# Optimization experiments

Hardware: AMD Instinct MI355X
Metric: run time of the kernel (lower is better)

## Reference

```python
import jax, jax.numpy as jnp
import numpy as np

N_NODES = 100000
N_EDGES = 250000
LATENT = 128
N_FEAT = 16
OUT = 128


def _mlp(x, W1, b1, W2, b2, W3, b3):
    # per-(class, port) MLP xi^{c,o}: two relu hidden layers, linear output
    h = jax.nn.relu(x @ W1 + b1)
    h = jax.nn.relu(h @ W2 + b2)
    return h @ W3 + b3


def setup_inputs() -> dict:
    key = jax.random.key(0)
    ks = jax.random.split(key, 12)
    d_in = 2 * LATENT + N_FEAT  # 272
    s = lambda k, shp, fan: jax.random.normal(k, shp, jnp.float32) / np.sqrt(fan)
    return {
        "coordinates": jax.random.normal(ks[0], (N_NODES, LATENT), jnp.float32),
        "edge_features": jax.random.normal(ks[1], (N_EDGES, N_FEAT), jnp.float32),
        "non_fictitious": jnp.ones((N_EDGES,), jnp.float32),
        "addr_port1": jax.random.randint(ks[2], (N_EDGES,), 0, N_NODES, jnp.int32),
        "addr_port2": jax.random.randint(ks[3], (N_EDGES,), 0, N_NODES, jnp.int32),
        "p1_W1": s(ks[4], (d_in, 256), d_in), "p1_b1": jnp.zeros((256,), jnp.float32),
        "p1_W2": s(ks[5], (256, 256), 256), "p1_b2": jnp.zeros((256,), jnp.float32),
        "p1_W3": s(ks[6], (256, OUT), 256), "p1_b3": jnp.zeros((OUT,), jnp.float32),
        "p2_W1": s(ks[7], (d_in, 256), d_in), "p2_b1": jnp.zeros((256,), jnp.float32),
        "p2_W2": s(ks[8], (256, 256), 256), "p2_b2": jnp.zeros((256,), jnp.float32),
        "p2_W3": s(ks[9], (256, OUT), 256), "p2_b3": jnp.zeros((OUT,), jnp.float32),
    }


def reference(coordinates, edge_features, non_fictitious, addr_port1, addr_port2,
              p1_W1, p1_b1, p1_W2, p1_b2, p1_W3, p1_b3,
              p2_W1, p2_b1, p2_W2, p2_b2, p2_W3, p2_b3):
    # Gather neighbor coordinates for each port and concat with edge features.
    # input_array: [n_edges, n_feat + 2*latent]
    inp = jnp.concatenate(
        [edge_features, coordinates[addr_port1], coordinates[addr_port2]], axis=-1)
    mask = non_fictitious[:, None]  # [n_edges, 1]

    acc = jnp.zeros((coordinates.shape[0], OUT), dtype=coordinates.dtype)
    # port 1 MLP -> scatter-add at port-1 addresses
    acc = acc.at[addr_port1].add(_mlp(inp, p1_W1, p1_b1, p1_W2, p1_b2, p1_W3, p1_b3) * mask)
    # port 2 MLP -> scatter-add at port-2 addresses
    acc = acc.at[addr_port2].add(_mlp(inp, p2_W1, p2_b1, p2_W2, p2_b2, p2_W3, p2_b3) * mask)
    return jnp.tanh(acc)
```

## Files before the change

### kernel.cpp

```cpp
#include <hip/hip_runtime.h>
#include <cstdint>

#define N_NODES 100000
#define N_EDGES_C 250000
#define LATENT 128
#define N_FEAT 16
#define OUT_DIM 128
#define D_IN 272
#define KC1 9
#define KC2 8
#define NT1 16
#define NT2 16
#define NT3 8
#define EPB 64
#define MT 4

#define SZ1 (KC1*NT1*512)
#define SZ2 (KC2*NT2*512)
#define SZ3 (KC2*NT3*512)
#define SZ_MLP (SZ1+SZ2+SZ3)
#define SZ_ALL (2*SZ_MLP)
#define WBLK (SZ_ALL/256)

#define NC4 (N_NODES*LATENT/4)
#define NE4 (N_EDGES_C*N_FEAT/4)
#define CBLK ((NC4+NE4+255)/256)

typedef _Float16 f16;
typedef _Float16 f16x8 __attribute__((ext_vector_type(8)));
typedef float f32x4 __attribute__((ext_vector_type(4)));
typedef unsigned short u16;
typedef u16 u16x8 __attribute__((ext_vector_type(8)));

__device__ u16 g_coords_h[(size_t)N_NODES * LATENT];
__device__ u16 g_efeat_h[(size_t)N_EDGES_C * N_FEAT];

static __device__ __forceinline__ u16 f16_bits(float v) {
    f16 h = (f16)v;
    return __builtin_bit_cast(u16, h);
}

__global__ void prep_all(const float* __restrict__ W1a, const float* __restrict__ W2a,
                         const float* __restrict__ W3a, const float* __restrict__ W1b,
                         const float* __restrict__ W2b, const float* __restrict__ W3b,
                         const float* __restrict__ coords, const float* __restrict__ efeat,
                         u16* __restrict__ Whi) {
    if (blockIdx.x < WBLK) {
        int idx = blockIdx.x * 256 + threadIdx.x;
        int mlp = idx / SZ_MLP;
        int r = idx - mlp * SZ_MLP;
        const float* Wsrc; int NT, Kreal, N, rl;
        if (r < SZ1)            { Wsrc = mlp ? W1b : W1a; NT = NT1; Kreal = D_IN; N = 256; rl = r; }
        else if (r < SZ1 + SZ2) { Wsrc = mlp ? W2b : W2a; NT = NT2; Kreal = 256;  N = 256; rl = r - SZ1; }
        else                    { Wsrc = mlp ? W3b : W3a; NT = NT3; Kreal = 256;  N = 128; rl = r - SZ1 - SZ2; }
        int block  = rl >> 9;
        int within = rl & 511;
        int quad = within >> 7;
        int nn   = (within >> 3) & 15;
        int j    = within & 7;
        int c = block / NT;
        int t = block - c * NT;
        int k = c * 32 + quad * 8 + j;
        int n = t * 16 + nn;
        float w = (k < Kreal) ? Wsrc[(size_t)k * N + n] : 0.f;
        Whi[idx] = f16_bits(w);
    } else {
        int i = (blockIdx.x - WBLK) * 256 + threadIdx.x;
        const float* src;
        u16* dst;
        if (i < NC4)               { src = coords + (size_t)i * 4; dst = g_coords_h + (size_t)i * 4; }
        else if (i < NC4 + NE4)    { int j = i - NC4; src = efeat + (size_t)j * 4; dst = g_efeat_h + (size_t)j * 4; }
        else return;
        f32x4 v = *(const f32x4*)src;
        ushort4 h;
        h.x = f16_bits(v.x); h.y = f16_bits(v.y);
        h.z = f16_bits(v.z); h.w = f16_bits(v.w);
        *(ushort4*)dst = h;
    }
}

static __device__ __forceinline__ void gatherX(u16* __restrict__ A,
                                               const int* __restrict__ pA,
                                               const int* __restrict__ pB,
                                               int ebase, int tid) {
    int m = tid >> 3;
    int p = tid & 7;
    int e = ebase + m;
    bool v = e < N_EDGES_C;
    int i1 = pA[m];
    int i2 = pB[m];
    const u16* ef = g_efeat_h + (size_t)e * N_FEAT;
    const u16* c1 = g_coords_h + (size_t)i1 * LATENT;
    const u16* c2 = g_coords_h + (size_t)i2 * LATENT;
    int mt = m >> 4, mr = m & 15;
    #pragma unroll
    for (int it = 0; it < 5; ++it) {
        int ci = p + it * 8;
        if (ci >= 36) break;
        int k = ci * 8;
        u16x8 h;
        if (!v || k >= D_IN)  h = (u16x8){0, 0, 0, 0, 0, 0, 0, 0};
        else if (k < 16)      h = __builtin_nontemporal_load((const u16x8*)(ef + k));
        else if (k < 144)     h = __builtin_nontemporal_load((const u16x8*)(c1 + (k - 16)));
        else                  h = __builtin_nontemporal_load((const u16x8*)(c2 + (k - 144)));
        int chunk = k >> 5, quad = (k >> 3) & 3;
        *(u16x8*)&A[(mt * KC1 + chunk) * 512 + quad * 128 + mr * 8] = h;
    }
}

template<int KCL, int KCA, int CT, int NTT>
static __device__ __forceinline__ void kloop(const u16* __restrict__ A,
                                             const u16* __restrict__ W,
                                             int w4, int lane,
                                             f32x4 (&acc)[MT][CT]) {
    const int la8 = lane * 8;
    const int tg0 = w4 * CT;
    u16x8 b[CT];
    #pragma unroll
    for (int t = 0; t < CT; ++t)
        b[t] = *(const u16x8*)&W[(tg0 + t) * 512 + la8];
    #pragma unroll
    for (int c = 0; c < KCL; ++c) {
        u16x8 bn[CT];
        if (c + 1 < KCL) {
            #pragma unroll
            for (int t = 0; t < CT; ++t)
                bn[t] = *(const u16x8*)&W[((c + 1) * NTT + tg0 + t) * 512 + la8];
        }
        f16x8 a[MT];
        #pragma unroll
        for (int mt = 0; mt < MT; ++mt)
            a[mt] = __builtin_bit_cast(f16x8, *(const u16x8*)&A[(mt * KCA + c) * 512 + la8]);
        #pragma unroll
        for (int t = 0; t < CT; ++t) {
            f16x8 bf = __builtin_bit_cast(f16x8, b[t]);
            #pragma unroll
            for (int mt = 0; mt < MT; ++mt)
                acc[mt][t] = __builtin_amdgcn_mfma_f32_16x16x32_f16(a[mt], bf, acc[mt][t], 0, 0, 0);
        }
        if (c + 1 < KCL) {
            #pragma unroll
            for (int t = 0; t < CT; ++t) b[t] = bn[t];
        }
    }
}

template<int KCL, int KCA, int CT, int NTT>
static __device__ __forceinline__ void layer_mm(const u16* __restrict__ A,
                                                const u16* __restrict__ W,
                                                int w4, int lane,
                                                f32x4 (&acc)[MT][CT]) {
    #pragma unroll
    for (int mt = 0; mt < MT; ++mt)
        #pragma unroll
        for (int t = 0; t < CT; ++t)
            acc[mt][t] = (f32x4){0.f, 0.f, 0.f, 0.f};
    kloop<KCL, KCA, CT, NTT>(A, W, w4, lane, acc);
}

template<int CT>
static __device__ __forceinline__ void epi_relu(u16* __restrict__ H,
                                                const float* __restrict__ bias,
                                                int w4, int lane,
                                                f32x4 (&acc)[MT][CT]) {
    int quad = lane >> 4, ln = lane & 15;
    #pragma unroll
    for (int t = 0; t < CT; ++t) {
        int n = (w4 * CT + t) * 16 + ln;
        float b = bias[n];
        int chunk = n >> 5, q2 = (n >> 3) & 3, j = n & 7;
        #pragma unroll
        for (int mt = 0; mt < MT; ++mt)
            #pragma unroll
            for (int r = 0; r < 4; ++r) {
                float v = acc[mt][t][r] + b;
                v = fmaxf(v, 0.f);
                H[(mt * KC2 + chunk) * 512 + q2 * 128 + (quad * 4 + r) * 8 + j] = f16_bits(v);
            }
    }
}

__global__ void __launch_bounds__(512, 4)
fused_mlp(const float* __restrict__ nfict,
          const int* __restrict__ port1, const int* __restrict__ port2,
          const float* __restrict__ b1a, const float* __restrict__ b2a, const float* __restrict__ b3a,
          const float* __restrict__ b1b, const float* __restrict__ b2b, const float* __restrict__ b3b,
          const u16* __restrict__ Whi,
          float* __restrict__ out) {
    __shared__ u16 X[MT * KC1 * 512];
    __shared__ u16 Ha[MT * KC2 * 512];
    __shared__ int pA[EPB], pB[EPB];
    __shared__ float mk[EPB];

    const int tid = threadIdx.x;
    const int lane = tid & 63;
    const int wave = tid >> 6;
    const int ebase = blockIdx.x * EPB;

    if (tid < EPB) {
        int e = ebase + tid;
        bool v = e < N_EDGES_C;
        pA[tid] = v ? port1[e] : 0;
        pB[tid] = v ? port2[e] : 0;
        mk[tid] = v ? nfict[e] : 0.f;
    }
    __syncthreads();
    gatherX(X, pA, pB, ebase, tid);
    __syncthreads();

    const int msel = wave >> 2;
    const int w4 = wave & 3;
    const u16* wh = Whi + msel * SZ_MLP;
    const float* B1 = msel ? b1b : b1a;
    const float* B2 = msel ? b2b : b2a;
    const float* B3 = msel ? b3b : b3a;
    const int*   pp = msel ? pB  : pA;
    u16* myH = msel ? X : Ha;

    f32x4 acc[MT][4];
    layer_mm<KC1, KC1, 4, NT1>(X, wh, w4, lane, acc);
    __syncthreads();
    epi_relu<4>(myH, B1, w4, lane, acc);
    __syncthreads();

    layer_mm<KC2, KC2, 4, NT2>(myH, wh + SZ1, w4, lane, acc);
    __syncthreads();
    epi_relu<4>(myH, B2, w4, lane, acc);
    __syncthreads();

    f32x4 acc3[MT][2];
    layer_mm<KC2, KC2, 2, NT3>(myH, wh + SZ1 + SZ2, w4, lane, acc3);

    int quad = lane >> 4, ln = lane & 15;
    #pragma unroll
    for (int t = 0; t < 2; ++t) {
        int n = (w4 * 2 + t) * 16 + ln;
        float bz = B3[n];
        #pragma unroll
        for (int mt = 0; mt < MT; ++mt)
            #pragma unroll
            for (int r = 0; r < 4; ++r) {
                int m = mt * 16 + quad * 4 + r;
                float v = (acc3[mt][t][r] + bz) * mk[m];
                unsafeAtomicAdd(out + (size_t)pp[m] * OUT_DIM + n, v);
            }
    }
}

__global__ void tanh_kernel(float* __restrict__ out, int n) {
    int i = (blockIdx.x * 256 + threadIdx.x) * 4;
    if (i + 3 < n) {
        float4 v = *(float4*)(out + i);
        v.x = tanhf(v.x); v.y = tanhf(v.y); v.z = tanhf(v.z); v.w = tanhf(v.w);
        *(float4*)(out + i) = v;
    } else {
        for (int k = i; k < n; ++k) out[k] = tanhf(out[k]);
    }
}

extern "C" void kernel_launch(void* const* d_in, const int* in_sizes, int n_in,
                              void* d_out, int out_size, void* d_ws, size_t ws_size,
                              hipStream_t stream) {
    const float* coords = (const float*)d_in[0];
    const float* efeat  = (const float*)d_in[1];
    const float* nfict  = (const float*)d_in[2];
    const int*   p1     = (const int*)d_in[3];
    const int*   p2     = (const int*)d_in[4];
    const float* W1a = (const float*)d_in[5];  const float* b1a = (const float*)d_in[6];
    const float* W2a = (const float*)d_in[7];  const float* b2a = (const float*)d_in[8];
    const float* W3a = (const float*)d_in[9];  const float* b3a = (const float*)d_in[10];
    const float* W1b = (const float*)d_in[11]; const float* b1b = (const float*)d_in[12];
    const float* W2b = (const float*)d_in[13]; const float* b2b = (const float*)d_in[14];
    const float* W3b = (const float*)d_in[15]; const float* b3b = (const float*)d_in[16];
    float* out = (float*)d_out;
    u16* Whi = (u16*)d_ws;

    hipMemsetAsync(d_out, 0, (size_t)out_size * sizeof(float), stream);
    prep_all<<<WBLK + CBLK, 256, 0, stream>>>(W1a, W2a, W3a, W1b, W2b, W3b,
                                              coords, efeat, Whi);
    int nblk = (N_EDGES_C + EPB - 1) / EPB;
    fused_mlp<<<nblk, 512, 0, stream>>>(nfict, p1, p2,
                                        b1a, b2a, b3a, b1b, b2b, b3b, Whi, out);
    int n4 = (out_size + 3) / 4;
    tanh_kernel<<<(n4 + 255) / 256, 256, 0, stream>>>(out, out_size);
}
```

Baseline: 499.4 us.

## Replace atomic scatter-add with CSR segmented reduction fused with tanh

The MLP kernel now writes per-edge messages to a global buffer instead of issuing float atomics into the output. A counting sort (count, single-block scan, fill) builds a per-node list of message rows, and a new kernel sums each node's messages with one wave per node and applies tanh, which replaces the memset and the separate tanh pass. This removes atomic contention and the extra output traffic. In exchange it writes and rereads about 256 MB of messages and adds several small launches, including a serial single-block scan.

```diff
diff --git a/kernel.cpp b/kernel.cpp
--- a/kernel.cpp
+++ b/kernel.cpp
@@ -25,6 +25,10 @@
 #define NC4 (N_NODES*LATENT/4)
 #define NE4 (N_EDGES_C*N_FEAT/4)
 #define CBLK ((NC4+NE4+255)/256)
+#define ZBLK ((N_NODES+255)/256)
+
+#define MSG_STRIDE 250048
+#define MSG_ROWS   (2*MSG_STRIDE)
 
 typedef _Float16 f16;
 typedef _Float16 f16x8 __attribute__((ext_vector_type(8)));
@@ -32,8 +36,13 @@
 typedef unsigned short u16;
 typedef u16 u16x8 __attribute__((ext_vector_type(8)));
 
-__device__ u16 g_coords_h[(size_t)N_NODES * LATENT];
-__device__ u16 g_efeat_h[(size_t)N_EDGES_C * N_FEAT];
+__device__ u16   g_coords_h[(size_t)N_NODES * LATENT];
+__device__ u16   g_efeat_h[(size_t)N_EDGES_C * N_FEAT];
+__device__ float g_msg[(size_t)MSG_ROWS * OUT_DIM];
+__device__ int   g_cnt[N_NODES];
+__device__ int   g_off[N_NODES];
+__device__ int   g_cur[N_NODES];
+__device__ int   g_eidx[2 * N_EDGES_C];
 
 static __device__ __forceinline__ u16 f16_bits(float v) {
     f16 h = (f16)v;
@@ -64,7 +73,7 @@
         int n = t * 16 + nn;
         float w = (k < Kreal) ? Wsrc[(size_t)k * N + n] : 0.f;
         Whi[idx] = f16_bits(w);
-    } else {
+    } else if (blockIdx.x < WBLK + CBLK) {
         int i = (blockIdx.x - WBLK) * 256 + threadIdx.x;
         const float* src;
         u16* dst;
@@ -76,7 +85,56 @@
         h.x = f16_bits(v.x); h.y = f16_bits(v.y);
         h.z = f16_bits(v.z); h.w = f16_bits(v.w);
         *(ushort4*)dst = h;
-    }
+    } else {
+        int i = (blockIdx.x - WBLK - CBLK) * 256 + threadIdx.x;
+        if (i < N_NODES) g_cnt[i] = 0;
+    }
+}
+
+__global__ void count_kernel(const int* __restrict__ port1, const int* __restrict__ port2) {
+    int i = blockIdx.x * 256 + threadIdx.x;
+    if (i >= 2 * N_EDGES_C) return;
+    int node = (i < N_EDGES_C) ? port1[i] : port2[i - N_EDGES_C];
+    atomicAdd(&g_cnt[node], 1);
+}
+
+__global__ void __launch_bounds__(1024) scan_kernel() {
+    __shared__ int s[1024];
+    const int t = threadIdx.x;
+    const int CH = (N_NODES + 1023) / 1024;
+    int base = t * CH;
+    int sum = 0;
+    for (int i = 0; i < CH; ++i) {
+        int idx = base + i;
+        if (idx < N_NODES) sum += g_cnt[idx];
+    }
+    s[t] = sum;
+    __syncthreads();
+    for (int off = 1; off < 1024; off <<= 1) {
+        int u = (t >= off) ? s[t - off] : 0;
+        __syncthreads();
+        s[t] += u;
+        __syncthreads();
+    }
+    int run = s[t] - sum;
+    for (int i = 0; i < CH; ++i) {
+        int idx = base + i;
+        if (idx < N_NODES) {
+            g_off[idx] = run;
+            g_cur[idx] = run;
+            run += g_cnt[idx];
+        }
+    }
+}
+
+__global__ void fill_kernel(const int* __restrict__ port1, const int* __restrict__ port2) {
+    int i = blockIdx.x * 256 + threadIdx.x;
+    if (i >= 2 * N_EDGES_C) return;
+    int node, row;
+    if (i < N_EDGES_C) { node = port1[i]; row = i; }
+    else               { node = port2[i - N_EDGES_C]; row = i + (MSG_STRIDE - N_EDGES_C); }
+    int pos = atomicAdd(&g_cur[node], 1);
+    g_eidx[pos] = row;
 }
 
 static __device__ __forceinline__ void gatherX(u16* __restrict__ A,
@@ -185,8 +243,7 @@
           const int* __restrict__ port1, const int* __restrict__ port2,
           const float* __restrict__ b1a, const float* __restrict__ b2a, const float* __restrict__ b3a,
           const float* __restrict__ b1b, const float* __restrict__ b2b, const float* __restrict__ b3b,
-          const u16* __restrict__ Whi,
-          float* __restrict__ out) {
+          const u16* __restrict__ Whi) {
     __shared__ u16 X[MT * KC1 * 512];
     __shared__ u16 Ha[MT * KC2 * 512];
     __shared__ int pA[EPB], pB[EPB];
@@ -214,7 +271,6 @@
     const float* B1 = msel ? b1b : b1a;
     const float* B2 = msel ? b2b : b2a;
     const float* B3 = msel ? b3b : b3a;
-    const int*   pp = msel ? pB  : pA;
     u16* myH = msel ? X : Ha;
 
     f32x4 acc[MT][4];
@@ -242,20 +298,29 @@
             for (int r = 0; r < 4; ++r) {
                 int m = mt * 16 + quad * 4 + r;
                 float v = (acc3[mt][t][r] + bz) * mk[m];
-                unsafeAtomicAdd(out + (size_t)pp[m] * OUT_DIM + n, v);
+                __builtin_nontemporal_store(v,
+                    &g_msg[(size_t)(msel * MSG_STRIDE + ebase + m) * OUT_DIM + n]);
             }
     }
 }
 
-__global__ void tanh_kernel(float* __restrict__ out, int n) {
-    int i = (blockIdx.x * 256 + threadIdx.x) * 4;
-    if (i + 3 < n) {
-        float4 v = *(float4*)(out + i);
-        v.x = tanhf(v.x); v.y = tanhf(v.y); v.z = tanhf(v.z); v.w = tanhf(v.w);
-        *(float4*)(out + i) = v;
-    } else {
-        for (int k = i; k < n; ++k) out[k] = tanhf(out[k]);
-    }
+__global__ void __launch_bounds__(256) scatter_sum(float* __restrict__ out) {
+    int w = (blockIdx.x * 256 + threadIdx.x) >> 6;
+    int lane = threadIdx.x & 63;
+    if (w >= N_NODES) return;
+    int off = g_off[w];
+    int cnt = g_cnt[w];
+    float ax = 0.f, ay = 0.f;
+    for (int j = 0; j < cnt; ++j) {
+        int row = g_eidx[off + j];
+        const float* p = &g_msg[(size_t)row * OUT_DIM + lane * 2];
+        float2 v = *(const float2*)p;
+        ax += v.x; ay += v.y;
+    }
+    float2 o;
+    o.x = tanhf(ax);
+    o.y = tanhf(ay);
+    *(float2*)&out[(size_t)w * OUT_DIM + lane * 2] = o;
 }
 
 extern "C" void kernel_launch(void* const* d_in, const int* in_sizes, int n_in,
@@ -275,12 +340,15 @@
     float* out = (float*)d_out;
     u16* Whi = (u16*)d_ws;
 
-    hipMemsetAsync(d_out, 0, (size_t)out_size * sizeof(float), stream);
-    prep_all<<<WBLK + CBLK, 256, 0, stream>>>(W1a, W2a, W3a, W1b, W2b, W3b,
-                                              coords, efeat, Whi);
+    prep_all<<<WBLK + CBLK + ZBLK, 256, 0, stream>>>(W1a, W2a, W3a, W1b, W2b, W3b,
+                                                     coords, efeat, Whi);
+    int cblk = (2 * N_EDGES_C + 255) / 256;
+    count_kernel<<<cblk, 256, 0, stream>>>(p1, p2);
+    scan_kernel<<<1, 1024, 0, stream>>>();
+    fill_kernel<<<cblk, 256, 0, stream>>>(p1, p2);
     int nblk = (N_EDGES_C + EPB - 1) / EPB;
     fused_mlp<<<nblk, 512, 0, stream>>>(nfict, p1, p2,
-                                        b1a, b2a, b3a, b1b, b2b, b3b, Whi, out);
-    int n4 = (out_size + 3) / 4;
-    tanh_kernel<<<(n4 + 255) / 256, 256, 0, stream>>>(out, out_size);
-}
+                                        b1a, b2a, b3a, b1b, b2b, b3b, Whi);
+    int sblk = (N_NODES * 64 + 255) / 256;
+    scatter_sum<<<sblk, 256, 0, stream>>>(out);
+}
```

Measured after the change: 891.8 us. 1.79x slower.

## Swizzle LDS activation layout, fold output zeroing into prep, drop gather sync

Applied to the files above, without the earlier changes.

Applies an XOR swizzle to the row index of the shared-memory activation tiles, both where the gather and ReLU epilogues write and where the MFMA A-fragments are read. The aim is to cut LDS bank conflicts, especially the scalar f16 stores in the epilogue. The output memset is folded into the prep kernel as extra blocks, which removes one launch. The gather now reads port indices straight from global memory, so one __syncthreads before it can go.

```diff
diff --git a/kernel.cpp b/kernel.cpp
--- a/kernel.cpp
+++ b/kernel.cpp
@@ -25,6 +25,8 @@
 #define NC4 (N_NODES*LATENT/4)
 #define NE4 (N_EDGES_C*N_FEAT/4)
 #define CBLK ((NC4+NE4+255)/256)
+#define NOUT4 (N_NODES*OUT_DIM/4)
+#define OBLK ((NOUT4+255)/256)
 
 typedef _Float16 f16;
 typedef _Float16 f16x8 __attribute__((ext_vector_type(8)));
@@ -40,11 +42,13 @@
     return __builtin_bit_cast(u16, h);
 }
 
+static __device__ __forceinline__ int swz(int s) { return s ^ ((s >> 2) & 6); }
+
 __global__ void prep_all(const float* __restrict__ W1a, const float* __restrict__ W2a,
                          const float* __restrict__ W3a, const float* __restrict__ W1b,
                          const float* __restrict__ W2b, const float* __restrict__ W3b,
                          const float* __restrict__ coords, const float* __restrict__ efeat,
-                         u16* __restrict__ Whi) {
+                         u16* __restrict__ Whi, float* __restrict__ outz) {
     if (blockIdx.x < WBLK) {
         int idx = blockIdx.x * 256 + threadIdx.x;
         int mlp = idx / SZ_MLP;
@@ -64,7 +68,7 @@
         int n = t * 16 + nn;
         float w = (k < Kreal) ? Wsrc[(size_t)k * N + n] : 0.f;
         Whi[idx] = f16_bits(w);
-    } else {
+    } else if (blockIdx.x < WBLK + CBLK) {
         int i = (blockIdx.x - WBLK) * 256 + threadIdx.x;
         const float* src;
         u16* dst;
@@ -76,19 +80,23 @@
         h.x = f16_bits(v.x); h.y = f16_bits(v.y);
         h.z = f16_bits(v.z); h.w = f16_bits(v.w);
         *(ushort4*)dst = h;
+    } else {
+        int i = (blockIdx.x - WBLK - CBLK) * 256 + threadIdx.x;
+        if (i < NOUT4)
+            *(f32x4*)&outz[(size_t)i * 4] = (f32x4){0.f, 0.f, 0.f, 0.f};
     }
 }
 
 static __device__ __forceinline__ void gatherX(u16* __restrict__ A,
-                                               const int* __restrict__ pA,
-                                               const int* __restrict__ pB,
+                                               const int* __restrict__ port1,
+                                               const int* __restrict__ port2,
                                                int ebase, int tid) {
     int m = tid >> 3;
     int p = tid & 7;
     int e = ebase + m;
     bool v = e < N_EDGES_C;
-    int i1 = pA[m];
-    int i2 = pB[m];
+    int i1 = v ? port1[e] : 0;
+    int i2 = v ? port2[e] : 0;
     const u16* ef = g_efeat_h + (size_t)e * N_FEAT;
     const u16* c1 = g_coords_h + (size_t)i1 * LATENT;
     const u16* c2 = g_coords_h + (size_t)i2 * LATENT;
@@ -104,7 +112,8 @@
         else if (k < 144)     h = __builtin_nontemporal_load((const u16x8*)(c1 + (k - 16)));
         else                  h = __builtin_nontemporal_load((const u16x8*)(c2 + (k - 144)));
         int chunk = k >> 5, quad = (k >> 3) & 3;
-        *(u16x8*)&A[(mt * KC1 + chunk) * 512 + quad * 128 + mr * 8] = h;
+        int s2 = swz(quad * 16 + mr);
+        *(u16x8*)&A[(mt * KC1 + chunk) * 512 + s2 * 8] = h;
     }
 }
 
@@ -114,6 +123,7 @@
                                              int w4, int lane,
                                              f32x4 (&acc)[MT][CT]) {
     const int la8 = lane * 8;
+    const int laA = swz(lane) * 8;
     const int tg0 = w4 * CT;
     u16x8 b[CT];
     #pragma unroll
@@ -130,7 +140,7 @@
         f16x8 a[MT];
         #pragma unroll
         for (int mt = 0; mt < MT; ++mt)
-            a[mt] = __builtin_bit_cast(f16x8, *(const u16x8*)&A[(mt * KCA + c) * 512 + la8]);
+            a[mt] = __builtin_bit_cast(f16x8, *(const u16x8*)&A[(mt * KCA + c) * 512 + laA]);
         #pragma unroll
         for (int t = 0; t < CT; ++t) {
             f16x8 bf = __builtin_bit_cast(f16x8, b[t]);
@@ -175,7 +185,8 @@
             for (int r = 0; r < 4; ++r) {
                 float v = acc[mt][t][r] + b;
                 v = fmaxf(v, 0.f);
-                H[(mt * KC2 + chunk) * 512 + q2 * 128 + (quad * 4 + r) * 8 + j] = f16_bits(v);
+                int s2 = swz(q2 * 16 + quad * 4 + r);
+                H[(mt * KC2 + chunk) * 512 + s2 * 8 + j] = f16_bits(v);
             }
     }
 }
@@ -204,8 +215,7 @@
         pB[tid] = v ? port2[e] : 0;
         mk[tid] = v ? nfict[e] : 0.f;
     }
-    __syncthreads();
-    gatherX(X, pA, pB, ebase, tid);
+    gatherX(X, port1, port2, ebase, tid);
     __syncthreads();
 
     const int msel = wave >> 2;
@@ -275,9 +285,8 @@
     float* out = (float*)d_out;
     u16* Whi = (u16*)d_ws;
 
-    hipMemsetAsync(d_out, 0, (size_t)out_size * sizeof(float), stream);
-    prep_all<<<WBLK + CBLK, 256, 0, stream>>>(W1a, W2a, W3a, W1b, W2b, W3b,
-                                              coords, efeat, Whi);
+    prep_all<<<WBLK + CBLK + OBLK, 256, 0, stream>>>(W1a, W2a, W3a, W1b, W2b, W3b,
+                                                     coords, efeat, Whi, out);
     int nblk = (N_EDGES_C + EPB - 1) / EPB;
     fused_mlp<<<nblk, 512, 0, stream>>>(nfict, p1, p2,
                                         b1a, b2a, b3a, b1b, b2b, b3b, Whi, out);
```

After: 510.9 us. +2.3%, slower.
